# Kernel optimization log

Hardware: AMD Instinct MI355X
Metric: run time of the kernel (lower is better)

Reference implementation:

```python
import jax, jax.numpy as jnp
import numpy as np

LN_EPS = 1e-5
OPM_EPS = 1e-3


def setup_inputs() -> dict:
    key = jax.random.key(0)
    ks = jax.random.split(key, 8)
    S, N, c_m, c_h, c_z = 128, 256, 256, 32, 128
    m = jax.random.normal(ks[0], (S, N, c_m), dtype=jnp.float32)
    mask = jnp.ones((S, N), dtype=jnp.float32)
    ln_w = jnp.ones((c_m,), dtype=jnp.float32)
    ln_b = jnp.zeros((c_m,), dtype=jnp.float32)
    sc1 = 1.0 / np.sqrt(c_m)
    w1 = jax.random.uniform(ks[1], (c_m, c_h), jnp.float32, -sc1, sc1)
    b1 = jax.random.uniform(ks[2], (c_h,), jnp.float32, -sc1, sc1)
    w2 = jax.random.uniform(ks[3], (c_m, c_h), jnp.float32, -sc1, sc1)
    b2 = jax.random.uniform(ks[4], (c_h,), jnp.float32, -sc1, sc1)
    sco = 1.0 / np.sqrt(c_h * c_h)
    wo = jax.random.uniform(ks[5], (c_h * c_h, c_z), jnp.float32, -sco, sco)
    bo = jax.random.uniform(ks[6], (c_z,), jnp.float32, -sco, sco)
    return {"m": m, "mask": mask, "ln_w": ln_w, "ln_b": ln_b,
            "w1": w1, "b1": b1, "w2": w2, "b2": b2, "wo": wo, "bo": bo}


def reference(m, mask, ln_w, ln_b, w1, b1, w2, b2, wo, bo):
    # LayerNorm over c_m
    mu = jnp.mean(m, axis=-1, keepdims=True)
    var = jnp.var(m, axis=-1, keepdims=True)
    ln = (m - mu) * jax.lax.rsqrt(var + LN_EPS) * ln_w + ln_b
    mk = mask[..., None]                       # [S, N, 1]
    a = (ln @ w1 + b1) * mk                    # [S, N, c_h]
    b = (ln @ w2 + b2) * mk                    # [S, N, c_h]
    # outer-product mean over the MSA dim s: [N, N, c_h, c_h]
    S, N, ch = a.shape
    outer = jnp.einsum('sic,sjd->ijcd', a, b).reshape(N, N, ch * ch)
    outer = outer @ wo + bo                    # [N, N, c_z]
    norm = jnp.einsum('si,sj->ij', mask, mask)[..., None] + OPM_EPS
    return outer / norm
```

## Files before the change

### kernel.cpp

```cpp
#include <hip/hip_runtime.h>
#include <hip/hip_bf16.h>

typedef __attribute__((ext_vector_type(8))) short short8;
typedef __attribute__((ext_vector_type(4))) short short4v;
typedef __attribute__((ext_vector_type(4))) float float4v;

#define S_DIM 128
#define N_DIM 256
#define CM    256
#define CH    32
#define CZ    128

static __device__ __forceinline__ short f2bf(float v) {
    return __builtin_bit_cast(short, __float2bfloat16(v));
}


__global__ __launch_bounds__(256) void prep_aux_kernel(
    const float* __restrict__ m, const float* __restrict__ mask,
    const float* __restrict__ lnw, const float* __restrict__ lnb,
    const float* __restrict__ w1, const float* __restrict__ b1,
    const float* __restrict__ w2, const float* __restrict__ b2,
    const float* __restrict__ wo, const float* __restrict__ bo,
    __hip_bfloat16* __restrict__ a_f, __hip_bfloat16* __restrict__ b_f,
    __hip_bfloat16* __restrict__ wo_f, float* __restrict__ ninv)
{
    __shared__ __align__(16) char lds_raw[77824];
    __hip_bfloat16* ln_lds = (__hip_bfloat16*)lds_raw;
    __hip_bfloat16* w_lds  = (__hip_bfloat16*)(lds_raw + 33792);
    __hip_bfloat16* st_lds = (__hip_bfloat16*)(lds_raw + 67584);

    const int bid = blockIdx.x, t = threadIdx.x;

    if (bid >= 576) {
        int i0 = (bid - 576) * 4, j = t;
        float a0 = 0.f, a1 = 0.f, a2 = 0.f, a3 = 0.f;
        for (int s = 0; s < S_DIM; ++s) {
            float mj = mask[s * N_DIM + j];
            a0 += mask[s * N_DIM + i0 + 0] * mj;
            a1 += mask[s * N_DIM + i0 + 1] * mj;
            a2 += mask[s * N_DIM + i0 + 2] * mj;
            a3 += mask[s * N_DIM + i0 + 3] * mj;
        }
        ninv[(i0 + 0) * N_DIM + j] = 1.0f / (a0 + 1e-3f);
        ninv[(i0 + 1) * N_DIM + j] = 1.0f / (a1 + 1e-3f);
        ninv[(i0 + 2) * N_DIM + j] = 1.0f / (a2 + 1e-3f);
        ninv[(i0 + 3) * N_DIM + j] = 1.0f / (a3 + 1e-3f);
        return;
    }
    if (bid >= 512) {
        int fidx = (bid - 512) * 256 + t;
        int l  = fidx & 63;
        int d  = (fidx >> 6) & 31;
        int zt = fidx >> 11;
        int z  = zt * 16 + (l & 15);
        int cb = (l >> 4) * 8;
        short8 frag;
        #pragma unroll
        for (int j = 0; j < 8; ++j)
            frag[j] = f2bf(wo[(size_t)((cb + j) * 32 + d) * CZ + z]);
        *(short8*)&wo_f[(size_t)fidx * 8] = frag;
        return;
    }

    const int lane = t & 63, wv = t >> 6;
    const int q = lane >> 4, c16 = lane & 15;
    const int n0 = (bid & 127) * 2, s0 = (bid >> 7) * 32, sk = bid >> 7;

    #pragma unroll 4
    for (int i = 0; i < 64; ++i) {
        int e = i * 256 + t;
        int k = e >> 6, c = e & 63;
        float v = (c < CH) ? w1[k * CH + c] : w2[k * CH + (c - CH)];
        w_lds[c * 264 + k] = __float2bfloat16(v);
    }

    float4 lw = ((const float4*)lnw)[lane];
    float4 lb = ((const float4*)lnb)[lane];

    #pragma unroll 2
    for (int it = 0; it < 16; ++it) {
        int rl = wv * 16 + it;
        int r  = (s0 + (rl >> 1)) * N_DIM + n0 + (rl & 1);
        float4 mv = ((const float4*)(m + (size_t)r * CM))[lane];
        float s1 = mv.x + mv.y + mv.z + mv.w;
        float s2 = mv.x*mv.x + mv.y*mv.y + mv.z*mv.z + mv.w*mv.w;
        #pragma unroll
        for (int o = 32; o > 0; o >>= 1) {
            s1 += __shfl_xor(s1, o, 64);
            s2 += __shfl_xor(s2, o, 64);
        }
        float mu  = s1 * (1.0f / 256.0f);
        float var = s2 * (1.0f / 256.0f) - mu * mu;
        float rs  = rsqrtf(var + 1e-5f);
        int base = rl * 264 + lane * 4;
        ln_lds[base + 0] = __float2bfloat16((mv.x - mu) * rs * lw.x + lb.x);
        ln_lds[base + 1] = __float2bfloat16((mv.y - mu) * rs * lw.y + lb.y);
        ln_lds[base + 2] = __float2bfloat16((mv.z - mu) * rs * lw.z + lb.z);
        ln_lds[base + 3] = __float2bfloat16((mv.w - mu) * rs * lw.w + lb.w);
    }
    __syncthreads();

    float4v acc[4];
    #pragma unroll
    for (int ct = 0; ct < 4; ++ct) acc[ct] = (float4v){0.f, 0.f, 0.f, 0.f};
    #pragma unroll
    for (int ks = 0; ks < 8; ++ks) {
        int k0 = ks * 32 + q * 8;
        short8 af = *(const short8*)&ln_lds[(wv * 16 + c16) * 264 + k0];
        #pragma unroll
        for (int ct = 0; ct < 4; ++ct) {
            short8 wb = *(const short8*)&w_lds[(ct * 16 + c16) * 264 + k0];
            acc[ct] = __builtin_amdgcn_mfma_f32_16x16x32_bf16(af, wb, acc[ct], 0, 0, 0);
        }
    }

    #pragma unroll
    for (int ct = 0; ct < 4; ++ct) {
        int cc = ct * 16 + c16;
        float bias = (cc < CH) ? b1[cc] : b2[cc - CH];
        #pragma unroll
        for (int rr = 0; rr < 4; ++rr) {
            int rl = wv * 16 + q * 4 + rr;
            int r  = (s0 + (rl >> 1)) * N_DIM + n0 + (rl & 1);
            float val = (acc[ct][rr] + bias) * mask[r];
            st_lds[((rl & 1) * 64 + cc) * 40 + (rl >> 1)] = __float2bfloat16(val);
        }
    }
    __syncthreads();

    #pragma unroll
    for (int i = 0; i < 2; ++i) {
        int slot = i * 256 + t;
        int f8 = slot >> 6, l = slot & 63;
        int fl = f8 & 3, nl = fl >> 1, cch = fl & 1;
        int lq = l >> 4, lc16 = l & 15;
        int col = nl * 64 + (f8 >= 4 ? 32 : 0) + cch * 16 + lc16;
        short8 v = *(const short8*)&st_lds[col * 40 + lq * 8];
        __hip_bfloat16* base = (f8 >= 4) ? b_f : a_f;
        *(short8*)&base[(size_t)((n0 * 2 + fl) * 4 + sk) * 512 + l * 8] = v;
    }
}

__global__ __launch_bounds__(512, 4) void main_kernel(
    const __hip_bfloat16* __restrict__ a_f, const __hip_bfloat16* __restrict__ b_f,
    const __hip_bfloat16* __restrict__ wo_f, const float* __restrict__ bo,
    const float* __restrict__ ninv, float* __restrict__ out)
{
    __shared__ __align__(16) short lds[33280];

    const int t = threadIdx.x, l = t & 63, wv = t >> 6;
    const int q = l >> 4, c16 = l & 15;
    const int bi = blockIdx.x, bj0 = blockIdx.y * 2;
    const int wr = wv & 3, wc = wv >> 2;
    const size_t Ix = (size_t)bi * 8;

    short8 af[4][2];
    #pragma unroll
    for (int sk = 0; sk < 4; ++sk)
        #pragma unroll
        for (int ti = 0; ti < 2; ++ti)
            af[sk][ti] = *(const short8*)&a_f[((Ix + wr * 2 + ti) * 4 + sk) * 512 + l * 8];

    #pragma unroll
    for (int tau = 0; tau < 2; ++tau) {
        const size_t Jx = (size_t)(bj0 + tau) * 8;
        float4v acc[2][4];
        #pragma unroll
        for (int ti = 0; ti < 2; ++ti)
            #pragma unroll
            for (int tj = 0; tj < 4; ++tj)
                acc[ti][tj] = (float4v){0.f, 0.f, 0.f, 0.f};

        #pragma unroll
        for (int st = 0; st < 2; ++st) {
            #pragma unroll
            for (int i = 0; i < 2; ++i) {
                int f  = i * 8 + wv;
                int xl = f >> 1, kk = f & 1;
                *(short8*)&lds[f * 512 + l * 8] =
                    *(const short8*)&b_f[((Jx + xl) * 4 + st * 2 + kk) * 512 + l * 8];
            }
            __syncthreads();
            #pragma unroll
            for (int kk = 0; kk < 2; ++kk) {
                short8 bf[4];
                #pragma unroll
                for (int tj = 0; tj < 4; ++tj)
                    bf[tj] = *(const short8*)&lds[((wc * 4 + tj) * 2 + kk) * 512 + l * 8];
                #pragma unroll
                for (int ti = 0; ti < 2; ++ti)
                    #pragma unroll
                    for (int tj = 0; tj < 4; ++tj)
                        acc[ti][tj] = __builtin_amdgcn_mfma_f32_16x16x32_bf16(
                            af[st * 2 + kk][ti], bf[tj], acc[ti][tj], 0, 0, 0);
            }
            __syncthreads();
        }

        const int pb = tau ? 0 : 16640;
        #pragma unroll
        for (int ti = 0; ti < 2; ++ti)
            #pragma unroll
            for (int tj = 0; tj < 4; ++tj) {
                int d  = ((tj & 1) * 16) + c16;
                int c0 = ti * 16 + q * 4;
                int p  = wr * 4 + wc * 2 + (tj >> 1);
                short4v pk;
                #pragma unroll
                for (int rr = 0; rr < 4; ++rr)
                    pk[rr] = f2bf(acc[ti][tj][rr]);
                *(short4v*)&lds[pb + d * 520 + (c0 >> 3) * 128 + p * 8 + (c0 & 7)] = pk;
            }
    }
    __syncthreads();

    float4v oacc[2];
    oacc[0] = (float4v){0.f, 0.f, 0.f, 0.f};
    oacc[1] = (float4v){0.f, 0.f, 0.f, 0.f};
    const __hip_bfloat16* wbase = wo_f + (size_t)wv * 32 * 512;
    short8 wA[4], wB[4];
    #pragma unroll
    for (int dd = 0; dd < 4; ++dd) {
        wA[dd] = *(const short8*)&wbase[(dd    ) * 512 + l * 8];
        wB[dd] = *(const short8*)&wbase[(dd + 4) * 512 + l * 8];
    }
    #pragma unroll
    for (int c = 0; c < 8; ++c) {
        #pragma unroll
        for (int dd = 0; dd < 4; ++dd) {
            int d = c * 4 + dd;
            short8 wf = (c & 1) ? wB[dd] : wA[dd];
            short8 p0 = *(const short8*)&lds[16640 + d * 520 + l * 8];
            short8 p1 = *(const short8*)&lds[        d * 520 + l * 8];
            if (c < 6) {
                short8 wn = *(const short8*)&wbase[(d + 8) * 512 + l * 8];
                if (c & 1) wB[dd] = wn; else wA[dd] = wn;
            }
            oacc[0] = __builtin_amdgcn_mfma_f32_16x16x32_bf16(p0, wf, oacc[0], 0, 0, 0);
            oacc[1] = __builtin_amdgcn_mfma_f32_16x16x32_bf16(p1, wf, oacc[1], 0, 0, 0);
        }
    }

    const int gi = bi * 4 + q;
    const int z  = wv * 16 + c16;
    const float bz = bo[z];
    #pragma unroll
    for (int tau = 0; tau < 2; ++tau) {
        const int bj = bj0 + tau;
        #pragma unroll
        for (int rr = 0; rr < 4; ++rr) {
            int gj = bj * 4 + rr;
            float nv = ninv[gi * N_DIM + gj];
            out[((size_t)gi * N_DIM + gj) * CZ + z] = (oacc[tau][rr] + bz) * nv;
        }
    }
}

extern "C" void kernel_launch(void* const* d_in, const int* in_sizes, int n_in,
                              void* d_out, int out_size, void* d_ws, size_t ws_size,
                              hipStream_t stream) {
    const float* m    = (const float*)d_in[0];
    const float* mask = (const float*)d_in[1];
    const float* lnw  = (const float*)d_in[2];
    const float* lnb  = (const float*)d_in[3];
    const float* w1   = (const float*)d_in[4];
    const float* b1   = (const float*)d_in[5];
    const float* w2   = (const float*)d_in[6];
    const float* b2   = (const float*)d_in[7];
    const float* wo   = (const float*)d_in[8];
    const float* bo   = (const float*)d_in[9];
    float* out = (float*)d_out;

    char* ws = (char*)d_ws;
    __hip_bfloat16* a_f  = (__hip_bfloat16*)ws;
    __hip_bfloat16* b_f  = (__hip_bfloat16*)(ws + (2u << 20));
    __hip_bfloat16* wo_f = (__hip_bfloat16*)(ws + (4u << 20));
    float*          ninv = (float*)(ws + (4u << 20) + (256u << 10));

    prep_aux_kernel<<<640, 256, 0, stream>>>(m, mask, lnw, lnb, w1, b1, w2, b2,
                                             wo, bo, a_f, b_f, wo_f, ninv);
    main_kernel<<<dim3(64, 32), 512, 0, stream>>>(a_f, b_f, wo_f, bo, ninv, out);
}
```

Baseline: 147.1 us.

## Halve main kernel LDS and process each j-tile end-to-end for higher occupancy

The main kernel now handles each of its two j-tiles fully before moving to the next. It loads all four k-slices of B into LDS at once, runs the outer-product MFMAs and stages the bf16 product. It then immediately runs the wo projection and writes that tile's output. This halves the LDS buffer and raises the launch-bounds occupancy hint from 4 to 6 blocks. The trade-off is that the wo fragments are reloaded from global memory for each tile instead of being shared across both, a-fragments are reloaded per tile, and the wo loads are no longer software-prefetched.

```diff
diff --git a/kernel.cpp b/kernel.cpp
--- a/kernel.cpp
+++ b/kernel.cpp
@@ -142,29 +142,42 @@
     }
 }
 
-__global__ __launch_bounds__(512, 4) void main_kernel(
+__global__ __launch_bounds__(512, 6) void main_kernel(
     const __hip_bfloat16* __restrict__ a_f, const __hip_bfloat16* __restrict__ b_f,
     const __hip_bfloat16* __restrict__ wo_f, const float* __restrict__ bo,
     const float* __restrict__ ninv, float* __restrict__ out)
 {
-    __shared__ __align__(16) short lds[33280];
+    __shared__ __align__(16) short lds[16640];
 
     const int t = threadIdx.x, l = t & 63, wv = t >> 6;
     const int q = l >> 4, c16 = l & 15;
     const int bi = blockIdx.x, bj0 = blockIdx.y * 2;
     const int wr = wv & 3, wc = wv >> 2;
     const size_t Ix = (size_t)bi * 8;
-
-    short8 af[4][2];
-    #pragma unroll
-    for (int sk = 0; sk < 4; ++sk)
-        #pragma unroll
-        for (int ti = 0; ti < 2; ++ti)
-            af[sk][ti] = *(const short8*)&a_f[((Ix + wr * 2 + ti) * 4 + sk) * 512 + l * 8];
+    const __hip_bfloat16* wbase = wo_f + (size_t)wv * 32 * 512;
+    const int gi = bi * 4 + q;
+    const int z  = wv * 16 + c16;
+    const float bz = bo[z];
 
     #pragma unroll
     for (int tau = 0; tau < 2; ++tau) {
         const size_t Jx = (size_t)(bj0 + tau) * 8;
+
+        #pragma unroll
+        for (int i = 0; i < 4; ++i) {
+            int f  = i * 8 + wv;
+            int xl = f >> 2, sk = f & 3;
+            *(short8*)&lds[f * 512 + l * 8] =
+                *(const short8*)&b_f[((Jx + xl) * 4 + sk) * 512 + l * 8];
+        }
+        short8 af[4][2];
+        #pragma unroll
+        for (int sk = 0; sk < 4; ++sk)
+            #pragma unroll
+            for (int ti = 0; ti < 2; ++ti)
+                af[sk][ti] = *(const short8*)&a_f[((Ix + wr * 2 + ti) * 4 + sk) * 512 + l * 8];
+        __syncthreads();
+
         float4v acc[2][4];
         #pragma unroll
         for (int ti = 0; ti < 2; ++ti)
@@ -173,32 +186,20 @@
                 acc[ti][tj] = (float4v){0.f, 0.f, 0.f, 0.f};
 
         #pragma unroll
-        for (int st = 0; st < 2; ++st) {
-            #pragma unroll
-            for (int i = 0; i < 2; ++i) {
-                int f  = i * 8 + wv;
-                int xl = f >> 1, kk = f & 1;
-                *(short8*)&lds[f * 512 + l * 8] =
-                    *(const short8*)&b_f[((Jx + xl) * 4 + st * 2 + kk) * 512 + l * 8];
-            }
-            __syncthreads();
-            #pragma unroll
-            for (int kk = 0; kk < 2; ++kk) {
-                short8 bf[4];
+        for (int sk = 0; sk < 4; ++sk) {
+            short8 bf[4];
+            #pragma unroll
+            for (int tj = 0; tj < 4; ++tj)
+                bf[tj] = *(const short8*)&lds[((wc * 4 + tj) * 4 + sk) * 512 + l * 8];
+            #pragma unroll
+            for (int ti = 0; ti < 2; ++ti)
                 #pragma unroll
                 for (int tj = 0; tj < 4; ++tj)
-                    bf[tj] = *(const short8*)&lds[((wc * 4 + tj) * 2 + kk) * 512 + l * 8];
-                #pragma unroll
-                for (int ti = 0; ti < 2; ++ti)
-                    #pragma unroll
-                    for (int tj = 0; tj < 4; ++tj)
-                        acc[ti][tj] = __builtin_amdgcn_mfma_f32_16x16x32_bf16(
-                            af[st * 2 + kk][ti], bf[tj], acc[ti][tj], 0, 0, 0);
-            }
-            __syncthreads();
-        }
-
-        const int pb = tau ? 0 : 16640;
+                    acc[ti][tj] = __builtin_amdgcn_mfma_f32_16x16x32_bf16(
+                        af[sk][ti], bf[tj], acc[ti][tj], 0, 0, 0);
+        }
+        __syncthreads();
+
         #pragma unroll
         for (int ti = 0; ti < 2; ++ti)
             #pragma unroll
@@ -210,50 +211,27 @@
                 #pragma unroll
                 for (int rr = 0; rr < 4; ++rr)
                     pk[rr] = f2bf(acc[ti][tj][rr]);
-                *(short4v*)&lds[pb + d * 520 + (c0 >> 3) * 128 + p * 8 + (c0 & 7)] = pk;
+                *(short4v*)&lds[d * 520 + (c0 >> 3) * 128 + p * 8 + (c0 & 7)] = pk;
             }
-    }
-    __syncthreads();
-
-    float4v oacc[2];
-    oacc[0] = (float4v){0.f, 0.f, 0.f, 0.f};
-    oacc[1] = (float4v){0.f, 0.f, 0.f, 0.f};
-    const __hip_bfloat16* wbase = wo_f + (size_t)wv * 32 * 512;
-    short8 wA[4], wB[4];
-    #pragma unroll
-    for (int dd = 0; dd < 4; ++dd) {
-        wA[dd] = *(const short8*)&wbase[(dd    ) * 512 + l * 8];
-        wB[dd] = *(const short8*)&wbase[(dd + 4) * 512 + l * 8];
-    }
-    #pragma unroll
-    for (int c = 0; c < 8; ++c) {
-        #pragma unroll
-        for (int dd = 0; dd < 4; ++dd) {
-            int d = c * 4 + dd;
-            short8 wf = (c & 1) ? wB[dd] : wA[dd];
-            short8 p0 = *(const short8*)&lds[16640 + d * 520 + l * 8];
-            short8 p1 = *(const short8*)&lds[        d * 520 + l * 8];
-            if (c < 6) {
-                short8 wn = *(const short8*)&wbase[(d + 8) * 512 + l * 8];
-                if (c & 1) wB[dd] = wn; else wA[dd] = wn;
-            }
-            oacc[0] = __builtin_amdgcn_mfma_f32_16x16x32_bf16(p0, wf, oacc[0], 0, 0, 0);
-            oacc[1] = __builtin_amdgcn_mfma_f32_16x16x32_bf16(p1, wf, oacc[1], 0, 0, 0);
-        }
-    }
-
-    const int gi = bi * 4 + q;
-    const int z  = wv * 16 + c16;
-    const float bz = bo[z];
-    #pragma unroll
-    for (int tau = 0; tau < 2; ++tau) {
+        __syncthreads();
+
+        float4v oacc = {0.f, 0.f, 0.f, 0.f};
+        #pragma unroll 4
+        for (int d = 0; d < 32; ++d) {
+            short8 pf = *(const short8*)&lds[d * 520 + l * 8];
+            short8 wf = *(const short8*)&wbase[(size_t)(d * 512 + l * 8)];
+            oacc = __builtin_amdgcn_mfma_f32_16x16x32_bf16(pf, wf, oacc, 0, 0, 0);
+        }
+
         const int bj = bj0 + tau;
         #pragma unroll
         for (int rr = 0; rr < 4; ++rr) {
             int gj = bj * 4 + rr;
             float nv = ninv[gi * N_DIM + gj];
-            out[((size_t)gi * N_DIM + gj) * CZ + z] = (oacc[tau][rr] + bz) * nv;
-        }
+            out[((size_t)gi * N_DIM + gj) * CZ + z] = (oacc[rr] + bz) * nv;
+        }
+
+        if (tau == 0) __syncthreads();
     }
 }
 
```

After: 181.5 us. 23.4% more time.
